# Optimization experiments

Measured on AMD Instinct MI355X. Metric: run time of the kernel, lower is better.

## Reference

```python
import jax, jax.numpy as jnp
import numpy as np
import math

# Model dims (from init_kwargs + mamba_ssm Mamba2 defaults)
D_MODEL = 1024
EXPAND = 2
HEADDIM = 64
D_STATE = 64
D_CONV = 4
NGROUPS = 1
D_INNER = EXPAND * D_MODEL            # 2048
NHEADS = D_INNER // HEADDIM           # 32
CONV_DIM = D_INNER + 2 * NGROUPS * D_STATE   # 2176
D_IN_PROJ = 2 * D_INNER + 2 * NGROUPS * D_STATE + NHEADS  # 4256
BATCH, SEQLEN = 4, 2048
RMS_EPS = 1.1920929e-07   # torch.finfo(float32).eps (nn.RMSNorm eps=None)
GNORM_EPS = 1e-5          # mamba_ssm RMSNormGated eps


def _rmsnorm(x, w, eps):
    return x * jax.lax.rsqrt(jnp.mean(x * x, axis=-1, keepdims=True) + eps) * w


def setup_inputs() -> dict:
    key = jax.random.key(0)
    ks = jax.random.split(key, 8)
    x = jax.random.normal(ks[0], (BATCH, SEQLEN, D_MODEL), jnp.float32)
    # router MLP (Linear(d_model,32) -> SiLU -> Linear(32,3))
    r_w1 = jax.random.normal(ks[1], (32, D_MODEL), jnp.float32) / math.sqrt(D_MODEL)
    r_b1 = jnp.zeros((32,), jnp.float32)
    r_w2 = jax.random.normal(ks[2], (3, 32), jnp.float32) / math.sqrt(32)
    r_b2 = jnp.zeros((3,), jnp.float32)
    # Mamba2 params
    in_proj_w = jax.random.normal(ks[3], (D_IN_PROJ, D_MODEL), jnp.float32) / math.sqrt(D_MODEL)
    conv_w = jax.random.normal(ks[4], (CONV_DIM, D_CONV), jnp.float32) * 0.2
    conv_b = jnp.zeros((CONV_DIM,), jnp.float32)
    dt_bias = jax.random.normal(ks[5], (NHEADS,), jnp.float32) * 0.1
    # OrthoSSM multi-scale override: A_log[i] = log(0.001 * 2**i)
    A_log = jnp.log(0.001 * (2.0 ** jnp.arange(NHEADS, dtype=jnp.float32)))
    D_param = jnp.ones((NHEADS,), jnp.float32)
    gnorm_w = jnp.ones((D_INNER,), jnp.float32)
    out_proj_w = jax.random.normal(ks[6], (D_MODEL, D_INNER), jnp.float32) / math.sqrt(D_INNER)
    norm_w = jnp.ones((D_MODEL,), jnp.float32)
    return {"x": x, "norm_w": norm_w, "r_w1": r_w1, "r_b1": r_b1, "r_w2": r_w2,
            "r_b2": r_b2, "in_proj_w": in_proj_w, "conv_w": conv_w, "conv_b": conv_b,
            "dt_bias": dt_bias, "A_log": A_log, "D_param": D_param,
            "gnorm_w": gnorm_w, "out_proj_w": out_proj_w}


def _forward(x, norm_w, r_w1, r_b1, r_w2, r_b2, in_proj_w, conv_w, conv_b,
             dt_bias, A_log, D_param, gnorm_w, out_proj_w):
    B, S, Dm = x.shape
    x_norm = _rmsnorm(x, norm_w, RMS_EPS)
    # --- router: mean-pool -> tiny MLP -> softmax over 3 tiers ---
    h = jax.nn.silu(x_norm.mean(axis=1) @ r_w1.T + r_b1)
    probs = jax.nn.softmax(h @ r_w2.T + r_b2, axis=-1)   # [B,3]
    p_fast = probs[:, 0][:, None, None]
    p_mamba = (probs[:, 1] + probs[:, 2])[:, None, None]
    # --- Mamba2(x_norm) ---
    zxbcdt = x_norm @ in_proj_w.T                         # [B,S,4256]
    z, xBC, dt = jnp.split(zxbcdt, [D_INNER, D_INNER + CONV_DIM], axis=-1)
    # causal depthwise conv1d (kernel 4) + SiLU
    conv = jax.lax.conv_general_dilated(
        xBC.transpose(0, 2, 1), conv_w[:, None, :], (1,), [(D_CONV - 1, 0)],
        feature_group_count=CONV_DIM)                      # [B,CONV_DIM,S]
    xBC = jax.nn.silu(conv.transpose(0, 2, 1) + conv_b)    # [B,S,CONV_DIM]
    xh, Bmat, Cmat = jnp.split(xBC, [D_INNER, D_INNER + NGROUPS * D_STATE], axis=-1)
    xh = xh.reshape(B, S, NHEADS, HEADDIM)                 # [B,S,H,P]
    dt = jax.nn.softplus(dt + dt_bias)                     # [B,S,H]
    A = -jnp.exp(A_log)                                    # [H]
    dA = jnp.exp(dt * A)                                   # [B,S,H]

    def step(hstate, inp):
        dA_t, dt_t, x_t, B_t, C_t = inp
        # hstate: [B,H,P,N]
        hstate = hstate * dA_t[..., None, None] \
                 + (dt_t[..., None] * x_t)[..., None] * B_t[:, None, None, :]
        y_t = jnp.einsum('bhpn,bn->bhp', hstate, C_t)
        return hstate, y_t

    h0 = jnp.zeros((B, NHEADS, HEADDIM, D_STATE), x.dtype)
    xs = (dA.transpose(1, 0, 2), dt.transpose(1, 0, 2), xh.transpose(1, 0, 2, 3),
          Bmat.transpose(1, 0, 2), Cmat.transpose(1, 0, 2))
    _, ys = jax.lax.scan(step, h0, xs)                     # [S,B,H,P]
    y = ys.transpose(1, 0, 2, 3) + D_param[:, None] * xh   # D skip connection
    y = y.reshape(B, S, D_INNER)
    # gated RMSNorm: norm(y * silu(z)) * weight
    yg = y * jax.nn.silu(z)
    yg = _rmsnorm(yg, gnorm_w, GNORM_EPS)
    mamba_out = yg @ out_proj_w.T                          # [B,S,D]
    out = p_fast * x_norm + p_mamba * mamba_out
    return x + out


def reference(x, norm_w, r_w1, r_b1, r_w2, r_b2, in_proj_w, conv_w, conv_b,
              dt_bias, A_log, D_param, gnorm_w, out_proj_w):
    return _forward(x, norm_w, r_w1, r_b1, r_w2, r_b2, in_proj_w, conv_w, conv_b,
                    dt_bias, A_log, D_param, gnorm_w, out_proj_w)
```

## Files before the change

### kernel.cpp

```cpp
#include <hip/hip_runtime.h>
#include <math.h>

typedef __bf16 bf16;
typedef __bf16 bf16x8 __attribute__((ext_vector_type(8)));
typedef __bf16 bf16x4 __attribute__((ext_vector_type(4)));
typedef float f32x4 __attribute__((ext_vector_type(4)));

#define DEV static __device__ __forceinline__
#define AS1 __attribute__((address_space(1)))
#define AS3 __attribute__((address_space(3)))

constexpr int kBatch = 4, kSeq = 2048, kDModel = 1024;
constexpr int kDInner = 2048, kHeads = 32;
constexpr int kConvDim = 2176, kDInProj = 4256, kNPad1 = 4352;
constexpr int kRows = kBatch * kSeq;
constexpr int kChunk = 64, kNChunk = kSeq / kChunk;
constexpr float kRmsEps = 1.1920929e-07f;
constexpr float kGnEps = 1e-5f;

DEV float siluf(float x) { return x / (1.f + expf(-x)); }

DEV float block_reduce_sum(float v, float* red, int tid) {
#pragma unroll
  for (int m = 1; m < 64; m <<= 1) v += __shfl_xor(v, m);
  if ((tid & 63) == 0) red[tid >> 6] = v;
  __syncthreads();
  return red[0] + red[1] + red[2] + red[3];
}

__global__ __launch_bounds__(256) void k_rmsnorm(const float* __restrict__ x,
                                                 const float* __restrict__ nw,
                                                 bf16* __restrict__ xnb) {
  const int row = blockIdx.x;
  const int tid = threadIdx.x;
  float4 v = ((const float4*)(x + (size_t)row * kDModel))[tid];
  __shared__ float red[4];
  float ss = block_reduce_sum(v.x * v.x + v.y * v.y + v.z * v.z + v.w * v.w, red, tid);
  float scale = rsqrtf(ss * (1.f / kDModel) + kRmsEps);
  float4 wv = ((const float4*)nw)[tid];
  bf16x4 ov;
  ov[0] = (bf16)(v.x * scale * wv.x);
  ov[1] = (bf16)(v.y * scale * wv.y);
  ov[2] = (bf16)(v.z * scale * wv.z);
  ov[3] = (bf16)(v.w * scale * wv.w);
  *(bf16x4*)(xnb + (size_t)row * kDModel + tid * 4) = ov;
}

__global__ __launch_bounds__(128) void k_pool1(const bf16* __restrict__ xnb,
                                               float* __restrict__ part) {
  const int g = blockIdx.x, b = blockIdx.y;
  const int tid = threadIdx.x;
  const bf16* base = xnb + ((size_t)b * kSeq + (size_t)g * 32) * kDModel + tid * 8;
  float acc[8] = {0, 0, 0, 0, 0, 0, 0, 0};
  for (int r = 0; r < 32; ++r) {
    bf16x8 v = *(const bf16x8*)(base + (size_t)r * kDModel);
#pragma unroll
    for (int j = 0; j < 8; ++j) acc[j] += (float)v[j];
  }
  float* o = part + ((size_t)b * 64 + g) * kDModel + tid * 8;
#pragma unroll
  for (int j = 0; j < 8; ++j) o[j] = acc[j];
}

__global__ __launch_bounds__(256) void k_pool2(const float* __restrict__ part,
                                               float* __restrict__ mean) {
  const int idx = blockIdx.x * 256 + threadIdx.x;
  const int b = idx >> 10, d = idx & 1023;
  float s = 0.f;
  for (int g = 0; g < 64; ++g) s += part[((size_t)b * 64 + g) * kDModel + d];
  mean[idx] = s * (1.f / kSeq);
}

__global__ __launch_bounds__(128) void k_router(const float* __restrict__ mean,
                                                const float* __restrict__ w1,
                                                const float* __restrict__ b1,
                                                const float* __restrict__ w2,
                                                const float* __restrict__ b2,
                                                float* __restrict__ pfm) {
  __shared__ float hbuf[4][32];
  __shared__ float logit[4][3];
  const int t = threadIdx.x;
  {
    int b = t >> 5, j = t & 31;
    float s = b1[j];
    for (int d = 0; d < kDModel; ++d) s += mean[b * kDModel + d] * w1[j * kDModel + d];
    hbuf[b][j] = siluf(s);
  }
  __syncthreads();
  if (t < 12) {
    int b = t / 3, k = t % 3;
    float s = b2[k];
    for (int j = 0; j < 32; ++j) s += hbuf[b][j] * w2[k * 32 + j];
    logit[b][k] = s;
  }
  __syncthreads();
  if (t < 4) {
    float m = fmaxf(logit[t][0], fmaxf(logit[t][1], logit[t][2]));
    float e0 = expf(logit[t][0] - m), e1 = expf(logit[t][1] - m), e2 = expf(logit[t][2] - m);
    float inv = 1.f / (e0 + e1 + e2);
    pfm[t] = e0 * inv;
    pfm[4 + t] = (e1 + e2) * inv;
  }
}

__global__ __launch_bounds__(256) void k_castpad_w1(const float* __restrict__ w,
                                                    bf16* __restrict__ wb) {
  const size_t idx = (size_t)blockIdx.x * 256 + threadIdx.x;
  const int row = (int)(idx >> 10);
  wb[idx] = (bf16)(row < kDInProj ? w[idx] : 0.f);
}

__global__ __launch_bounds__(256) void k_cast_w2(const float* __restrict__ w,
                                                 bf16* __restrict__ wb) {
  const size_t i4 = (size_t)blockIdx.x * 256 + threadIdx.x;
  float4 v = ((const float4*)w)[i4];
  bf16x4 o;
  o[0] = (bf16)v.x; o[1] = (bf16)v.y; o[2] = (bf16)v.z; o[3] = (bf16)v.w;
  ((bf16x4*)wb)[i4] = o;
}

template <int WM, int WN, int NF>
__global__ __launch_bounds__(WM * WN * 64, 4) void k_gemm(
    const bf16* __restrict__ A, const bf16* __restrict__ B,
    bf16* __restrict__ Cb, int K, int Nreal, int ldc, int ntn) {
  constexpr int THREADS = WM * WN * 64;
  constexpr int BM = WM * 64;
  constexpr int BN = WN * NF * 16;
  constexpr int NA = (BM * 4) / THREADS;
  constexpr int NB = (BN * 4) / THREADS;
  __shared__ __align__(16) bf16 Al[2][BM / 2][64];
  __shared__ __align__(16) bf16 Bl[2][BN / 2][64];
  const int tid = threadIdx.x;
  const int lane = tid & 63, wid = tid >> 6;
  const int wr = wid / WN, wc = wid % WN;
  const int lr = lane & 15, kb = lane >> 4;
  const int cpx = (int)gridDim.x >> 3;
  const int bid = ((int)blockIdx.x & 7) * cpx + ((int)blockIdx.x >> 3);
  const long n0 = (long)(bid % ntn) * BN;
  const long m0 = (long)(bid / ntn) * BM;

  f32x4 acc[4][NF];
#pragma unroll
  for (int i = 0; i < 4; ++i)
#pragma unroll
    for (int j = 0; j < NF; ++j) acc[i][j] = (f32x4){0.f, 0.f, 0.f, 0.f};

  const int nkt = K >> 5;

#define STAGE(pp, kt)                                                          \
  {                                                                            \
    const long koff = (long)(kt)*32;                                           \
    _Pragma("unroll") for (int j = 0; j < NA; ++j) {                           \
      int idx = j * THREADS + tid;                                             \
      int line = idx >> 3, sp = (idx & 7) ^ (line & 7);                        \
      int row = line * 2 + (sp >> 2), ch = sp & 3;                             \
      __builtin_amdgcn_global_load_lds(                                        \
          (const AS1 void*)(A + (m0 + row) * K + koff + ch * 8),               \
          (AS3 void*)((char*)&Al[pp][0][0] + idx * 16), 16, 0, 0);             \
    }                                                                          \
    _Pragma("unroll") for (int j = 0; j < NB; ++j) {                           \
      int idx = j * THREADS + tid;                                             \
      int line = idx >> 3, sp = (idx & 7) ^ (line & 7);                        \
      int row = line * 2 + (sp >> 2), ch = sp & 3;                             \
      __builtin_amdgcn_global_load_lds(                                        \
          (const AS1 void*)(B + (n0 + row) * K + koff + ch * 8),               \
          (AS3 void*)((char*)&Bl[pp][0][0] + idx * 16), 16, 0, 0);             \
    }                                                                          \
  }
#define LOFF(r) (((r) >> 1) * 128 + (((((r)&1) << 2) | kb) ^ (((r) >> 1) & 7)) * 16)
#define RDA(pp, r) (*(const bf16x8*)((const char*)&Al[pp][0][0] + LOFF(r)))
#define RDB(pp, r) (*(const bf16x8*)((const char*)&Bl[pp][0][0] + LOFF(r)))

  bf16x8 bfr[NF];
  bf16x8 af[2];

  STAGE(0, 0);
  __syncthreads();
#pragma unroll
  for (int nf = 0; nf < NF; ++nf) bfr[nf] = RDB(0, wc * 64 + nf * 16 + lr);
  af[0] = RDA(0, wr * 64 + lr);

  for (int t = 0; t < nkt; ++t) {
    const int p = t & 1;
    if (t + 1 < nkt) STAGE(p ^ 1, t + 1);
#pragma unroll
    for (int q = 0; q < 4; ++q) {
      if (q < 3) af[(q + 1) & 1] = RDA(p, wr * 64 + (q + 1) * 16 + lr);
      __builtin_amdgcn_s_setprio(1);
#pragma unroll
      for (int nf = 0; nf < NF; ++nf)
        acc[q][nf] = __builtin_amdgcn_mfma_f32_16x16x32_bf16(af[q & 1], bfr[nf],
                                                             acc[q][nf], 0, 0, 0);
      __builtin_amdgcn_s_setprio(0);
    }
    if (t + 1 < nkt) {
      __syncthreads();
#pragma unroll
      for (int nf = 0; nf < NF; ++nf) bfr[nf] = RDB(p ^ 1, wc * 64 + nf * 16 + lr);
      af[0] = RDA(p ^ 1, wr * 64 + lr);
    }
  }
#undef STAGE
#undef LOFF
#undef RDA
#undef RDB

  const int rr = kb * 4;
#pragma unroll
  for (int mf = 0; mf < 4; ++mf) {
#pragma unroll
    for (int nf = 0; nf < NF; ++nf) {
      int col = (int)n0 + wc * 64 + nf * 16 + lr;
      if (col < Nreal) {
        long rbase = m0 + wr * 64 + mf * 16 + rr;
#pragma unroll
        for (int j = 0; j < 4; ++j)
          Cb[(rbase + j) * (long)ldc + col] = (bf16)acc[mf][nf][j];
      }
    }
  }
}

__global__ __launch_bounds__(256) void k_conv(const bf16* __restrict__ zx,
                                              const float* __restrict__ cw,
                                              const float* __restrict__ cb,
                                              bf16* __restrict__ xbc) {
  const int gid = blockIdx.x * 256 + threadIdx.x;
  if (gid >= kRows * 272) return;
  const int row = gid / 272;
  const int cg = gid - row * 272;
  const int c0 = cg * 8;
  const int s = row & (kSeq - 1);
  const bf16* base = zx + (size_t)row * kDInProj + kDInner + c0;
  bf16x8 z8 = {};
  bf16x8 r3 = *(const bf16x8*)(base);
  bf16x8 r2 = (s >= 1) ? *(const bf16x8*)(base - kDInProj) : z8;
  bf16x8 r1 = (s >= 2) ? *(const bf16x8*)(base - 2 * kDInProj) : z8;
  bf16x8 r0 = (s >= 3) ? *(const bf16x8*)(base - 3 * kDInProj) : z8;
  bf16x8 o;
#pragma unroll
  for (int e = 0; e < 8; ++e) {
    float4 w = ((const float4*)cw)[c0 + e];
    float a = cb[c0 + e] + w.x * (float)r0[e] + w.y * (float)r1[e] +
              w.z * (float)r2[e] + w.w * (float)r3[e];
    o[e] = (bf16)siluf(a);
  }
  *(bf16x8*)(xbc + (size_t)row * kConvDim + c0) = o;
}

__global__ __launch_bounds__(256) void k_dtda(const bf16* __restrict__ zx,
                                              const float* __restrict__ dt_bias,
                                              const float* __restrict__ A_log,
                                              float* __restrict__ dt, float* __restrict__ ldA) {
  const int idx = blockIdx.x * 256 + threadIdx.x;
  const int row = idx >> 5, hh = idx & 31;
  float raw = (float)zx[(size_t)row * kDInProj + (kDInner + kConvDim) + hh] + dt_bias[hh];
  float dtv = (raw > 20.f) ? raw : log1pf(expf(raw));
  dt[idx] = dtv;
  ldA[idx] = dtv * -expf(A_log[hh]);
}

__global__ __launch_bounds__(256) void k_chunkA(
    const bf16* __restrict__ xbc, const float* __restrict__ dtb,
    const float* __restrict__ ldab, float* __restrict__ cumbuf,
    float* __restrict__ Tc, bf16* __restrict__ yb, bf16* __restrict__ Sbuf) {
  const int c = blockIdx.x, h = blockIdx.y, b = blockIdx.z;
  const int tid = threadIdx.x;
  const int w = tid >> 6, lane = tid & 63, lr = lane & 15, kb = lane >> 4;
  const int rr = kb * 4;
  const int t0 = c * kChunk;
  __shared__ bf16 Bl[64 * 72], Cl[64 * 72], XT[64 * 72], WBT[64 * 72], Ml[64 * 72];
  __shared__ float cum_s[64], dt_s[64], w_s[64];

  {
    int s = tid >> 2, q = tid & 3;
    const bf16* rowp = xbc + ((size_t)b * kSeq + t0 + s) * kConvDim;
    bf16x8 x0 = *(const bf16x8*)(rowp + h * 64 + q * 16);
    bf16x8 x1 = *(const bf16x8*)(rowp + h * 64 + q * 16 + 8);
    bf16x8 b0 = *(const bf16x8*)(rowp + kDInner + q * 16);
    bf16x8 b1 = *(const bf16x8*)(rowp + kDInner + q * 16 + 8);
    bf16x8 c0 = *(const bf16x8*)(rowp + kDInner + 64 + q * 16);
    bf16x8 c1 = *(const bf16x8*)(rowp + kDInner + 64 + q * 16 + 8);
    *(bf16x8*)(Bl + s * 72 + q * 16) = b0;
    *(bf16x8*)(Bl + s * 72 + q * 16 + 8) = b1;
    *(bf16x8*)(Cl + s * 72 + q * 16) = c0;
    *(bf16x8*)(Cl + s * 72 + q * 16 + 8) = c1;
#pragma unroll
    for (int e = 0; e < 8; ++e) XT[(q * 16 + e) * 72 + s] = x0[e];
#pragma unroll
    for (int e = 0; e < 8; ++e) XT[(q * 16 + 8 + e) * 72 + s] = x1[e];
  }
  if (tid < 64) {
    size_t di = ((size_t)b * kSeq + t0 + tid) * kHeads + h;
    float v = ldab[di];
    float dtv = dtb[di];
#pragma unroll
    for (int o = 1; o < 64; o <<= 1) {
      float u = __shfl_up(v, o);
      if (lane >= o) v += u;
    }
    cum_s[tid] = v;
    dt_s[tid] = dtv;
    float tot = __shfl(v, 63);
    w_s[tid] = expf(tot - v) * dtv;
    cumbuf[(((size_t)b * kHeads + h) * kNChunk + c) * 64 + tid] = v;
    if (tid == 63) Tc[(b * kHeads + h) * kNChunk + c] = expf(v);
  }
  __syncthreads();

#pragma unroll
  for (int i = 0; i < 16; ++i) {
    int e = i * 256 + tid;
    int n = e >> 6, s = e & 63;
    WBT[n * 72 + s] = (bf16)((float)Bl[s * 72 + n] * w_s[s]);
  }

  f32x4 g[4];
#pragma unroll
  for (int nt = 0; nt < 4; ++nt) g[nt] = (f32x4){0.f, 0.f, 0.f, 0.f};
#pragma unroll
  for (int kk = 0; kk < 2; ++kk) {
    bf16x8 a = *(const bf16x8*)(Cl + (w * 16 + lr) * 72 + kk * 32 + kb * 8);
#pragma unroll
    for (int nt = 0; nt < 4; ++nt) {
      bf16x8 bb = *(const bf16x8*)(Bl + (nt * 16 + lr) * 72 + kk * 32 + kb * 8);
      g[nt] = __builtin_amdgcn_mfma_f32_16x16x32_bf16(a, bb, g[nt], 0, 0, 0);
    }
  }
#pragma unroll
  for (int nt = 0; nt < 4; ++nt)
#pragma unroll
    for (int j = 0; j < 4; ++j) {
      int tt = w * 16 + rr + j, ss = nt * 16 + lr;
      float m = (ss <= tt) ? g[nt][j] * expf(cum_s[tt] - cum_s[ss]) * dt_s[ss] : 0.f;
      Ml[tt * 72 + ss] = (bf16)m;
    }
  __syncthreads();

  f32x4 y4[4];
#pragma unroll
  for (int pt = 0; pt < 4; ++pt) y4[pt] = (f32x4){0.f, 0.f, 0.f, 0.f};
#pragma unroll
  for (int kk = 0; kk < 2; ++kk) {
    bf16x8 a = *(const bf16x8*)(Ml + (w * 16 + lr) * 72 + kk * 32 + kb * 8);
#pragma unroll
    for (int pt = 0; pt < 4; ++pt) {
      bf16x8 bb = *(const bf16x8*)(XT + (pt * 16 + lr) * 72 + kk * 32 + kb * 8);
      y4[pt] = __builtin_amdgcn_mfma_f32_16x16x32_bf16(a, bb, y4[pt], 0, 0, 0);
    }
  }
#pragma unroll
  for (int pt = 0; pt < 4; ++pt)
#pragma unroll
    for (int j = 0; j < 4; ++j) {
      int tt = w * 16 + rr + j, pp = pt * 16 + lr;
      yb[((size_t)b * kSeq + t0 + tt) * kDInner + h * 64 + pp] = (bf16)y4[pt][j];
    }

  f32x4 s4[4];
#pragma unroll
  for (int nt = 0; nt < 4; ++nt) s4[nt] = (f32x4){0.f, 0.f, 0.f, 0.f};
#pragma unroll
  for (int kk = 0; kk < 2; ++kk) {
    bf16x8 a = *(const bf16x8*)(XT + (w * 16 + lr) * 72 + kk * 32 + kb * 8);
#pragma unroll
    for (int nt = 0; nt < 4; ++nt) {
      bf16x8 bb = *(const bf16x8*)(WBT + (nt * 16 + lr) * 72 + kk * 32 + kb * 8);
      s4[nt] = __builtin_amdgcn_mfma_f32_16x16x32_bf16(a, bb, s4[nt], 0, 0, 0);
    }
  }
  const size_t sbase = (((size_t)b * kHeads + h) * kNChunk + c) * 4096;
#pragma unroll
  for (int nt = 0; nt < 4; ++nt)
#pragma unroll
    for (int j = 0; j < 4; ++j) {
      int pp = w * 16 + rr + j, nn = nt * 16 + lr;
      Sbuf[sbase + pp * 64 + nn] = (bf16)s4[nt][j];
    }
}

__global__ __launch_bounds__(256) void k_chunkB(bf16* __restrict__ S,
                                                const float* __restrict__ Tc) {
  const int gid = blockIdx.x * 256 + threadIdx.x;
  const int bh = gid >> 10;
  const int pn = (gid & 1023) << 2;
  bf16* base = S + (size_t)bh * kNChunk * 4096 + pn;
  const float* tc = Tc + bh * kNChunk;
  float4 hh = {0.f, 0.f, 0.f, 0.f};
  bf16x4 s = *(const bf16x4*)(base);
  for (int c = 0; c < kNChunk; ++c) {
    bf16x4 sn = {};
    if (c + 1 < kNChunk) sn = *(const bf16x4*)(base + (size_t)(c + 1) * 4096);
    float t = tc[c];
    bf16x4 ho;
    ho[0] = (bf16)hh.x; ho[1] = (bf16)hh.y; ho[2] = (bf16)hh.z; ho[3] = (bf16)hh.w;
    *(bf16x4*)(base + (size_t)c * 4096) = ho;
    hh.x = t * hh.x + (float)s[0];
    hh.y = t * hh.y + (float)s[1];
    hh.z = t * hh.z + (float)s[2];
    hh.w = t * hh.w + (float)s[3];
    s = sn;
  }
}

__global__ __launch_bounds__(256) void k_chunkC(
    const bf16* __restrict__ xbc, const float* __restrict__ cumbuf,
    const bf16* __restrict__ hs, const float* __restrict__ Dp,
    bf16* __restrict__ yb) {
  const int c = blockIdx.x, h = blockIdx.y, b = blockIdx.z;
  const int tid = threadIdx.x;
  const int w = tid >> 6, lane = tid & 63, lr = lane & 15, kb = lane >> 4;
  const int rr = kb * 4;
  const int t0 = c * kChunk;
  __shared__ bf16 Cl[64 * 72];
  __shared__ float ecum[64];
  {
    int s = tid >> 2, q = tid & 3;
    const bf16* rowp = xbc + ((size_t)b * kSeq + t0 + s) * kConvDim + kDInner + 64 + q * 16;
    *(bf16x8*)(Cl + s * 72 + q * 16) = *(const bf16x8*)rowp;
    *(bf16x8*)(Cl + s * 72 + q * 16 + 8) = *(const bf16x8*)(rowp + 8);
  }
  if (tid < 64)
    ecum[tid] = expf(cumbuf[(((size_t)b * kHeads + h) * kNChunk + c) * 64 + tid]);
  __syncthreads();

  const bf16* hbase = hs + (((size_t)b * kHeads + h) * kNChunk + c) * 4096;
  f32x4 acc[4];
#pragma unroll
  for (int pt = 0; pt < 4; ++pt) acc[pt] = (f32x4){0.f, 0.f, 0.f, 0.f};
#pragma unroll
  for (int kk = 0; kk < 2; ++kk) {
    bf16x8 a = *(const bf16x8*)(Cl + (w * 16 + lr) * 72 + kk * 32 + kb * 8);
#pragma unroll
    for (int pt = 0; pt < 4; ++pt) {
      bf16x8 bb = *(const bf16x8*)(hbase + (pt * 16 + lr) * 64 + kk * 32 + kb * 8);
      acc[pt] = __builtin_amdgcn_mfma_f32_16x16x32_bf16(a, bb, acc[pt], 0, 0, 0);
    }
  }
  const float Dh = Dp[h];
#pragma unroll
  for (int pt = 0; pt < 4; ++pt)
#pragma unroll
    for (int j = 0; j < 4; ++j) {
      int tt = w * 16 + rr + j, pp = pt * 16 + lr;
      size_t ri = (size_t)b * kSeq + t0 + tt;
      size_t yi = ri * kDInner + h * 64 + pp;
      float xv = (float)xbc[ri * kConvDim + h * 64 + pp];
      yb[yi] = (bf16)((float)yb[yi] + ecum[tt] * acc[pt][j] + Dh * xv);
    }
}

__global__ __launch_bounds__(256) void k_gnorm(const bf16* __restrict__ y,
                                               const bf16* __restrict__ zx,
                                               const float* __restrict__ gw,
                                               bf16* __restrict__ yg) {
  const int row = blockIdx.x;
  const int tid = threadIdx.x;
  const int c0 = tid * 8;
  bf16x8 yv = *(const bf16x8*)(y + (size_t)row * kDInner + c0);
  bf16x8 zv = *(const bf16x8*)(zx + (size_t)row * kDInProj + c0);
  float v[8];
  float ss = 0.f;
#pragma unroll
  for (int j = 0; j < 8; ++j) {
    float val = (float)yv[j] * siluf((float)zv[j]);
    v[j] = val;
    ss += val * val;
  }
  __shared__ float red[4];
  ss = block_reduce_sum(ss, red, tid);
  float scale = rsqrtf(ss * (1.f / kDInner) + kGnEps);
  bf16x8 ov;
#pragma unroll
  for (int j = 0; j < 8; ++j) ov[j] = (bf16)(v[j] * scale * gw[c0 + j]);
  *(bf16x8*)(yg + (size_t)row * kDInner + c0) = ov;
}

__global__ __launch_bounds__(256) void k_combine(const float* __restrict__ x,
                                                 const float* __restrict__ nw,
                                                 const bf16* __restrict__ mo,
                                                 const float* __restrict__ pfm,
                                                 float* __restrict__ out) {
  const int row = blockIdx.x;
  const int tid = threadIdx.x;
  const int b = row >> 11;
  float4 v = ((const float4*)(x + (size_t)row * kDModel))[tid];
  __shared__ float red[4];
  float ss = block_reduce_sum(v.x * v.x + v.y * v.y + v.z * v.z + v.w * v.w, red, tid);
  float scale = rsqrtf(ss * (1.f / kDModel) + kRmsEps);
  float pf = pfm[b], pm = pfm[4 + b];
  float4 wv = ((const float4*)nw)[tid];
  bf16x4 mv = *(const bf16x4*)(mo + (size_t)row * kDModel + tid * 4);
  float4 o;
  o.x = v.x + pf * (v.x * scale * wv.x) + pm * (float)mv[0];
  o.y = v.y + pf * (v.y * scale * wv.y) + pm * (float)mv[1];
  o.z = v.z + pf * (v.z * scale * wv.z) + pm * (float)mv[2];
  o.w = v.w + pf * (v.w * scale * wv.w) + pm * (float)mv[3];
  ((float4*)(out + (size_t)row * kDModel))[tid] = o;
}

extern "C" void kernel_launch(void* const* d_in, const int* in_sizes, int n_in,
                              void* d_out, int out_size, void* d_ws, size_t ws_size,
                              hipStream_t stream) {
  const float* x = (const float*)d_in[0];
  const float* norm_w = (const float*)d_in[1];
  const float* r_w1 = (const float*)d_in[2];
  const float* r_b1 = (const float*)d_in[3];
  const float* r_w2 = (const float*)d_in[4];
  const float* r_b2 = (const float*)d_in[5];
  const float* in_proj_w = (const float*)d_in[6];
  const float* conv_w = (const float*)d_in[7];
  const float* conv_b = (const float*)d_in[8];
  const float* dt_bias = (const float*)d_in[9];
  const float* A_log = (const float*)d_in[10];
  const float* D_param = (const float*)d_in[11];
  const float* gnorm_w = (const float*)d_in[12];
  const float* out_proj_w = (const float*)d_in[13];
  float* out = (float*)d_out;
  char* ws = (char*)d_ws;

  bf16* xnb     = (bf16*)(ws + 0);
  bf16* w1b     = (bf16*)(ws + 16777216);
  bf16* zx      = (bf16*)(ws + 25690112);
  bf16* xbc     = (bf16*)(ws + 95420416);
  float* dtb    = (float*)(ws + 131072000);
  float* ldab   = (float*)(ws + 132120576);
  float* cumbuf = (float*)(ws + 133169152);
  float* Tcb    = (float*)(ws + 134217728);
  bf16* yb      = (bf16*)(ws + 134234112);
  bf16* Sbuf    = (bf16*)(ws + 167788544);
  bf16* yg      = (bf16*)(ws + 167788544);
  bf16* w2b     = (bf16*)(ws + 201342976);
  float* part   = (float*)(ws + 205537280);
  float* meanb  = (float*)(ws + 206585856);
  float* pfm    = (float*)(ws + 206602240);
  bf16* mo      = (bf16*)(ws + 95420416);

  k_rmsnorm<<<kRows, 256, 0, stream>>>(x, norm_w, xnb);
  k_pool1<<<dim3(64, 4), 128, 0, stream>>>(xnb, part);
  k_pool2<<<16, 256, 0, stream>>>(part, meanb);
  k_router<<<1, 128, 0, stream>>>(meanb, r_w1, r_b1, r_w2, r_b2, pfm);
  k_castpad_w1<<<kNPad1 * kDModel / 256, 256, 0, stream>>>(in_proj_w, w1b);
  k_cast_w2<<<kDModel * kDInner / 1024, 256, 0, stream>>>(out_proj_w, w2b);
  k_gemm<2, 4, 4><<<(kRows / 128) * (kNPad1 / 256), 512, 0, stream>>>(
      xnb, w1b, zx, kDModel, kDInProj, kDInProj, kNPad1 / 256);
  k_conv<<<kRows * 272 / 256, 256, 0, stream>>>(zx, conv_w, conv_b, xbc);
  k_dtda<<<kRows * kHeads / 256, 256, 0, stream>>>(zx, dt_bias, A_log, dtb, ldab);
  k_chunkA<<<dim3(kNChunk, kHeads, kBatch), 256, 0, stream>>>(
      xbc, dtb, ldab, cumbuf, Tcb, yb, Sbuf);
  k_chunkB<<<512, 256, 0, stream>>>(Sbuf, Tcb);
  k_chunkC<<<dim3(kNChunk, kHeads, kBatch), 256, 0, stream>>>(
      xbc, cumbuf, Sbuf, D_param, yb);
  k_gnorm<<<kRows, 256, 0, stream>>>(yb, zx, gnorm_w, yg);
  k_gemm<2, 2, 4><<<(kRows / 128) * (kDModel / 128), 256, 0, stream>>>(
      yg, w2b, mo, kDInner, kDModel, kDModel, kDModel / 128);
  k_combine<<<kRows, 256, 0, stream>>>(x, norm_w, mo, pfm, out);
}
```

Measured before the change: 355.5 us.

## Triple-buffer GEMM loads and fuse final residual combine into out-proj GEMM

The GEMM main loop moves from double-buffered LDS with a full __syncthreads per tile to a three-stage ring. Loads run two tiles ahead, guarded by explicit vmcnt waits and raw s_barrier. The out-projection GEMM epilogue now computes the residual combine directly (x + pf*rmsnorm(x) + pm*acc) in fp32 using per-row scales saved by k_rmsnorm. This removes the separate combine kernel, the bf16 round trip of the mamba output, and the row-norm recomputation. The cost is more LDS per block, which may lower occupancy, plus uncoalesced strided fp32 reads and writes in the fused epilogue.

Measured after the change: 362.1 us. Within noise of the previous version (+1.9%).

```diff
diff --git a/kernel.cpp b/kernel.cpp
--- a/kernel.cpp
+++ b/kernel.cpp
@@ -30,13 +30,15 @@
 
 __global__ __launch_bounds__(256) void k_rmsnorm(const float* __restrict__ x,
                                                  const float* __restrict__ nw,
-                                                 bf16* __restrict__ xnb) {
+                                                 bf16* __restrict__ xnb,
+                                                 float* __restrict__ rs) {
   const int row = blockIdx.x;
   const int tid = threadIdx.x;
   float4 v = ((const float4*)(x + (size_t)row * kDModel))[tid];
   __shared__ float red[4];
   float ss = block_reduce_sum(v.x * v.x + v.y * v.y + v.z * v.z + v.w * v.w, red, tid);
   float scale = rsqrtf(ss * (1.f / kDModel) + kRmsEps);
+  if (tid == 0) rs[row] = scale;
   float4 wv = ((const float4*)nw)[tid];
   bf16x4 ov;
   ov[0] = (bf16)(v.x * scale * wv.x);
@@ -119,17 +121,21 @@
   ((bf16x4*)wb)[i4] = o;
 }
 
-template <int WM, int WN, int NF>
+template <int WM, int WN, int NF, bool FUSE>
 __global__ __launch_bounds__(WM * WN * 64, 4) void k_gemm(
     const bf16* __restrict__ A, const bf16* __restrict__ B,
-    bf16* __restrict__ Cb, int K, int Nreal, int ldc, int ntn) {
+    bf16* __restrict__ Cb, const float* __restrict__ xres,
+    const float* __restrict__ rs, const float* __restrict__ nw,
+    const float* __restrict__ pfm, float* __restrict__ outf,
+    int K, int Nreal, int ldc, int ntn) {
   constexpr int THREADS = WM * WN * 64;
   constexpr int BM = WM * 64;
   constexpr int BN = WN * NF * 16;
   constexpr int NA = (BM * 4) / THREADS;
   constexpr int NB = (BN * 4) / THREADS;
-  __shared__ __align__(16) bf16 Al[2][BM / 2][64];
-  __shared__ __align__(16) bf16 Bl[2][BN / 2][64];
+  constexpr int VMN = NA + NB;
+  __shared__ __align__(16) bf16 Al[3][BM / 2][64];
+  __shared__ __align__(16) bf16 Bl[3][BN / 2][64];
   const int tid = threadIdx.x;
   const int lane = tid & 63, wid = tid >> 6;
   const int wr = wid / WN, wc = wid % WN;
@@ -170,52 +176,85 @@
 #define LOFF(r) (((r) >> 1) * 128 + (((((r)&1) << 2) | kb) ^ (((r) >> 1) & 7)) * 16)
 #define RDA(pp, r) (*(const bf16x8*)((const char*)&Al[pp][0][0] + LOFF(r)))
 #define RDB(pp, r) (*(const bf16x8*)((const char*)&Bl[pp][0][0] + LOFF(r)))
-
-  bf16x8 bfr[NF];
-  bf16x8 af[2];
+#define WAIT_VMN()                                                             \
+  if constexpr (VMN == 3) asm volatile("s_waitcnt vmcnt(3)" ::: "memory");     \
+  else asm volatile("s_waitcnt vmcnt(4)" ::: "memory");
 
   STAGE(0, 0);
-  __syncthreads();
-#pragma unroll
-  for (int nf = 0; nf < NF; ++nf) bfr[nf] = RDB(0, wc * 64 + nf * 16 + lr);
-  af[0] = RDA(0, wr * 64 + lr);
-
+  STAGE(1, 1);
+  WAIT_VMN();
+  __builtin_amdgcn_s_barrier();
+
+  int cur = 0;
   for (int t = 0; t < nkt; ++t) {
-    const int p = t & 1;
-    if (t + 1 < nkt) STAGE(p ^ 1, t + 1);
-#pragma unroll
-    for (int q = 0; q < 4; ++q) {
-      if (q < 3) af[(q + 1) & 1] = RDA(p, wr * 64 + (q + 1) * 16 + lr);
-      __builtin_amdgcn_s_setprio(1);
+    int sb = cur + 2; if (sb >= 3) sb -= 3;
+    if (t + 2 < nkt) {
+      STAGE(sb, t + 2);
+      WAIT_VMN();
+    } else {
+      asm volatile("s_waitcnt vmcnt(0)" ::: "memory");
+    }
+    __builtin_amdgcn_s_barrier();
+
+    bf16x8 af[4], bv[NF];
+#pragma unroll
+    for (int mf = 0; mf < 4; ++mf) af[mf] = RDA(cur, wr * 64 + mf * 16 + lr);
+#pragma unroll
+    for (int nf = 0; nf < NF; ++nf) bv[nf] = RDB(cur, wc * 64 + nf * 16 + lr);
+    asm volatile("s_waitcnt lgkmcnt(0)" ::: "memory");
+    __builtin_amdgcn_sched_barrier(0);
+    __builtin_amdgcn_s_barrier();
+
+    __builtin_amdgcn_s_setprio(1);
+#pragma unroll
+    for (int mf = 0; mf < 4; ++mf)
 #pragma unroll
       for (int nf = 0; nf < NF; ++nf)
-        acc[q][nf] = __builtin_amdgcn_mfma_f32_16x16x32_bf16(af[q & 1], bfr[nf],
-                                                             acc[q][nf], 0, 0, 0);
-      __builtin_amdgcn_s_setprio(0);
-    }
-    if (t + 1 < nkt) {
-      __syncthreads();
-#pragma unroll
-      for (int nf = 0; nf < NF; ++nf) bfr[nf] = RDB(p ^ 1, wc * 64 + nf * 16 + lr);
-      af[0] = RDA(p ^ 1, wr * 64 + lr);
-    }
+        acc[mf][nf] = __builtin_amdgcn_mfma_f32_16x16x32_bf16(af[mf], bv[nf],
+                                                              acc[mf][nf], 0, 0, 0);
+    __builtin_amdgcn_s_setprio(0);
+    cur = cur + 1 == 3 ? 0 : cur + 1;
   }
 #undef STAGE
 #undef LOFF
 #undef RDA
 #undef RDB
+#undef WAIT_VMN
 
   const int rr = kb * 4;
-#pragma unroll
-  for (int mf = 0; mf < 4; ++mf) {
-#pragma unroll
-    for (int nf = 0; nf < NF; ++nf) {
-      int col = (int)n0 + wc * 64 + nf * 16 + lr;
-      if (col < Nreal) {
-        long rbase = m0 + wr * 64 + mf * 16 + rr;
-#pragma unroll
-        for (int j = 0; j < 4; ++j)
-          Cb[(rbase + j) * (long)ldc + col] = (bf16)acc[mf][nf][j];
+  if constexpr (FUSE) {
+    const int bx = (int)(m0 >> 11);
+    const float pf = pfm[bx], pm = pfm[4 + bx];
+#pragma unroll
+    for (int mf = 0; mf < 4; ++mf) {
+      long rbase = m0 + wr * 64 + mf * 16 + rr;
+      float rsv[4];
+#pragma unroll
+      for (int j = 0; j < 4; ++j) rsv[j] = rs[rbase + j];
+#pragma unroll
+      for (int nf = 0; nf < NF; ++nf) {
+        int col = (int)n0 + wc * 64 + nf * 16 + lr;
+        float wv = nw[col];
+#pragma unroll
+        for (int j = 0; j < 4; ++j) {
+          size_t oi = (size_t)(rbase + j) * kDModel + col;
+          float xv = xres[oi];
+          outf[oi] = xv + pf * xv * rsv[j] * wv + pm * acc[mf][nf][j];
+        }
+      }
+    }
+  } else {
+#pragma unroll
+    for (int mf = 0; mf < 4; ++mf) {
+#pragma unroll
+      for (int nf = 0; nf < NF; ++nf) {
+        int col = (int)n0 + wc * 64 + nf * 16 + lr;
+        if (col < Nreal) {
+          long rbase = m0 + wr * 64 + mf * 16 + rr;
+#pragma unroll
+          for (int j = 0; j < 4; ++j)
+            Cb[(rbase + j) * (long)ldc + col] = (bf16)acc[mf][nf][j];
+        }
       }
     }
   }
@@ -476,29 +515,6 @@
   *(bf16x8*)(yg + (size_t)row * kDInner + c0) = ov;
 }
 
-__global__ __launch_bounds__(256) void k_combine(const float* __restrict__ x,
-                                                 const float* __restrict__ nw,
-                                                 const bf16* __restrict__ mo,
-                                                 const float* __restrict__ pfm,
-                                                 float* __restrict__ out) {
-  const int row = blockIdx.x;
-  const int tid = threadIdx.x;
-  const int b = row >> 11;
-  float4 v = ((const float4*)(x + (size_t)row * kDModel))[tid];
-  __shared__ float red[4];
-  float ss = block_reduce_sum(v.x * v.x + v.y * v.y + v.z * v.z + v.w * v.w, red, tid);
-  float scale = rsqrtf(ss * (1.f / kDModel) + kRmsEps);
-  float pf = pfm[b], pm = pfm[4 + b];
-  float4 wv = ((const float4*)nw)[tid];
-  bf16x4 mv = *(const bf16x4*)(mo + (size_t)row * kDModel + tid * 4);
-  float4 o;
-  o.x = v.x + pf * (v.x * scale * wv.x) + pm * (float)mv[0];
-  o.y = v.y + pf * (v.y * scale * wv.y) + pm * (float)mv[1];
-  o.z = v.z + pf * (v.z * scale * wv.z) + pm * (float)mv[2];
-  o.w = v.w + pf * (v.w * scale * wv.w) + pm * (float)mv[3];
-  ((float4*)(out + (size_t)row * kDModel))[tid] = o;
-}
-
 extern "C" void kernel_launch(void* const* d_in, const int* in_sizes, int n_in,
                               void* d_out, int out_size, void* d_ws, size_t ws_size,
                               hipStream_t stream) {
@@ -534,16 +550,17 @@
   float* part   = (float*)(ws + 205537280);
   float* meanb  = (float*)(ws + 206585856);
   float* pfm    = (float*)(ws + 206602240);
-  bf16* mo      = (bf16*)(ws + 95420416);
-
-  k_rmsnorm<<<kRows, 256, 0, stream>>>(x, norm_w, xnb);
+  float* rsb    = (float*)(ws + 206602368);
+
+  k_rmsnorm<<<kRows, 256, 0, stream>>>(x, norm_w, xnb, rsb);
   k_pool1<<<dim3(64, 4), 128, 0, stream>>>(xnb, part);
   k_pool2<<<16, 256, 0, stream>>>(part, meanb);
   k_router<<<1, 128, 0, stream>>>(meanb, r_w1, r_b1, r_w2, r_b2, pfm);
   k_castpad_w1<<<kNPad1 * kDModel / 256, 256, 0, stream>>>(in_proj_w, w1b);
   k_cast_w2<<<kDModel * kDInner / 1024, 256, 0, stream>>>(out_proj_w, w2b);
-  k_gemm<2, 4, 4><<<(kRows / 128) * (kNPad1 / 256), 512, 0, stream>>>(
-      xnb, w1b, zx, kDModel, kDInProj, kDInProj, kNPad1 / 256);
+  k_gemm<2, 4, 4, false><<<(kRows / 128) * (kNPad1 / 256), 512, 0, stream>>>(
+      xnb, w1b, zx, nullptr, nullptr, nullptr, nullptr, nullptr,
+      kDModel, kDInProj, kDInProj, kNPad1 / 256);
   k_conv<<<kRows * 272 / 256, 256, 0, stream>>>(zx, conv_w, conv_b, xbc);
   k_dtda<<<kRows * kHeads / 256, 256, 0, stream>>>(zx, dt_bias, A_log, dtb, ldab);
   k_chunkA<<<dim3(kNChunk, kHeads, kBatch), 256, 0, stream>>>(
@@ -552,7 +569,7 @@
   k_chunkC<<<dim3(kNChunk, kHeads, kBatch), 256, 0, stream>>>(
       xbc, cumbuf, Sbuf, D_param, yb);
   k_gnorm<<<kRows, 256, 0, stream>>>(yb, zx, gnorm_w, yg);
-  k_gemm<2, 2, 4><<<(kRows / 128) * (kDModel / 128), 256, 0, stream>>>(
-      yg, w2b, mo, kDInner, kDModel, kDModel, kDModel / 128);
-  k_combine<<<kRows, 256, 0, stream>>>(x, norm_w, mo, pfm, out);
-}
+  k_gemm<2, 2, 4, true><<<(kRows / 128) * (kDModel / 128), 256, 0, stream>>>(
+      yg, w2b, nullptr, x, rsb, norm_w, pfm, out,
+      kDInner, kDModel, kDModel, kDModel / 128);
+}
```
